# Kernel tuning notes

Measured on AMD Instinct MI355X. Metric: run time of the kernel, lower is better.

## Reference

```python
import jax, jax.numpy as jnp
import numpy as np

N_HEAD = 12
D_HEAD = 64  # inner_dim 768 / 12 heads

def quick_gelu(x):
    return x * jax.nn.sigmoid(1.702 * x)

def setup_inputs() -> dict:
    key = jax.random.key(0)
    ks = jax.random.split(key, 12)
    B, Nv, Lt, Cv, Ct, Ci = 256, 196, 32, 768, 512, 768
    s = lambda k, shp, fan: jax.random.normal(k, shp, jnp.float32) / np.sqrt(fan)
    return {
        "vis_tokens": jax.random.normal(ks[0], (B, Nv, Cv), jnp.float32),
        "text_tokens": jax.random.normal(ks[1], (B, Lt, Ct), jnp.float32),
        "Wq": s(ks[2], (Cv, Ci), Cv), "bq": jnp.zeros((Ci,), jnp.float32),
        "Wk": s(ks[3], (Ct, Ci), Ct), "bk": jnp.zeros((Ci,), jnp.float32),
        "Wv": s(ks[4], (Ct, Ci), Ct), "bv": jnp.zeros((Ci,), jnp.float32),
        "W1": s(ks[5], (Ci, Ci), Ci), "b1": jnp.zeros((Ci,), jnp.float32),
        "W2": s(ks[6], (Ci, 2), Ci), "b2": jnp.zeros((2,), jnp.float32),
    }

def reference(vis_tokens, text_tokens, Wq, bq, Wk, bk, Wv, bv, W1, b1, W2, b2):
    B, Nv, _ = vis_tokens.shape
    Lt = text_tokens.shape[1]
    Ci = Wq.shape[1]
    # projections -> [B, H, N, D]
    q = (vis_tokens @ Wq + bq).reshape(B, Nv, N_HEAD, D_HEAD).transpose(0, 2, 1, 3)
    k = (text_tokens @ Wk + bk).reshape(B, Lt, N_HEAD, D_HEAD).transpose(0, 2, 1, 3)
    v = (text_tokens @ Wv + bv).reshape(B, Lt, N_HEAD, D_HEAD).transpose(0, 2, 1, 3)
    scores = jnp.einsum('bhnd,bhld->bhnl', q, k) / np.sqrt(D_HEAD).astype(np.float32)
    attn = jax.nn.softmax(scores, axis=-1)           # [B,H,Nv,Lt]
    ctx = jnp.einsum('bhnl,bhld->bhnd', attn, v)      # [B,H,Nv,D]
    ctx = ctx.transpose(0, 2, 1, 3).reshape(B, Nv, Ci)
    fused = ctx + vis_tokens[..., :Ci]
    logits = quick_gelu(fused @ W1 + b1) @ W2 + b2    # [B,Nv,2]
    rel_BN = attn.mean(axis=-1).mean(axis=1)          # [B,Nv]
    return (logits, rel_BN)
```

## Files before the change

kernel.cpp:

```cpp
#include <hip/hip_runtime.h>
#include <hip/hip_bf16.h>


typedef __attribute__((ext_vector_type(8))) short bf16x8;
typedef __attribute__((ext_vector_type(4))) float f32x4;

__device__ __forceinline__ float bf2f(unsigned short u) {
    return __uint_as_float(((unsigned int)u) << 16);
}
__device__ __forceinline__ unsigned short f2bf(float f) {
    unsigned int x = __float_as_uint(f);
    unsigned int r = (x + 0x7FFFu + ((x >> 16) & 1u)) >> 16;
    return (unsigned short)r;
}

__global__ void cvt_bf16_kernel(const float* __restrict__ in,
                                unsigned short* __restrict__ out, int n4) {
    int i = blockIdx.x * 256 + threadIdx.x;
    if (i >= n4) return;
    float4 v = ((const float4*)in)[i];
    ushort4 o;
    o.x = f2bf(v.x); o.y = f2bf(v.y); o.z = f2bf(v.z); o.w = f2bf(v.w);
    ((ushort4*)out)[i] = o;
}

__global__ void transpose_cvt_kernel(const float* __restrict__ W,
                                     unsigned short* __restrict__ Wt,
                                     int K, int N) {
    __shared__ float tile[32][33];
    int n0 = blockIdx.x * 32, k0 = blockIdx.y * 32;
    int tx = threadIdx.x & 31, ty = threadIdx.x >> 5;
    #pragma unroll
    for (int r = ty; r < 32; r += 8)
        tile[r][tx] = W[(size_t)(k0 + r) * N + n0 + tx];
    __syncthreads();
    #pragma unroll
    for (int r = ty; r < 32; r += 8)
        Wt[(size_t)(n0 + r) * K + k0 + tx] = f2bf(tile[tx][r]);
}

template<int KTOT, int GELU>
__global__ __launch_bounds__(256, 2)
void gemm_bt_kernel(const unsigned short* __restrict__ A,
                    const unsigned short* __restrict__ Bt,
                    const float* __restrict__ bias,
                    unsigned short* __restrict__ C) {
    constexpr int LDSW = 72;
    __shared__ unsigned short As[128 * LDSW];
    __shared__ unsigned short Bs[128 * LDSW];
    const int tid = threadIdx.x;
    const size_t m0 = (size_t)blockIdx.y * 128;
    const int n0 = blockIdx.x * 128;
    const int lane = tid & 63;
    const int wave = tid >> 6;
    const int wm = (wave >> 1) * 64;
    const int wn = (wave & 1) * 64;
    const int lr = lane & 15;
    const int quad = lane >> 4;

    f32x4 acc[4][4] = {};

    for (int kt = 0; kt < KTOT; kt += 64) {
        #pragma unroll
        for (int i = 0; i < 4; ++i) {
            int c = tid + i * 256;
            int r = c >> 3, col = (c & 7) * 8;
            bf16x8 v = *(const bf16x8*)(A + (m0 + r) * KTOT + kt + col);
            *(bf16x8*)(As + r * LDSW + col) = v;
        }
        #pragma unroll
        for (int i = 0; i < 4; ++i) {
            int c = tid + i * 256;
            int r = c >> 3, col = (c & 7) * 8;
            bf16x8 v = *(const bf16x8*)(Bt + (size_t)(n0 + r) * KTOT + kt + col);
            *(bf16x8*)(Bs + r * LDSW + col) = v;
        }
        __syncthreads();
        #pragma unroll
        for (int kk = 0; kk < 64; kk += 32) {
            bf16x8 fa[4], fb[4];
            #pragma unroll
            for (int i = 0; i < 4; ++i)
                fa[i] = *(const bf16x8*)(As + (wm + i * 16 + lr) * LDSW + kk + quad * 8);
            #pragma unroll
            for (int j = 0; j < 4; ++j)
                fb[j] = *(const bf16x8*)(Bs + (wn + j * 16 + lr) * LDSW + kk + quad * 8);
            #pragma unroll
            for (int i = 0; i < 4; ++i)
                #pragma unroll
                for (int j = 0; j < 4; ++j)
                    acc[i][j] = __builtin_amdgcn_mfma_f32_16x16x32_bf16(
                        fa[i], fb[j], acc[i][j], 0, 0, 0);
        }
        __syncthreads();
    }

    #pragma unroll
    for (int j = 0; j < 4; ++j) {
        int col = n0 + wn + j * 16 + lr;
        float bv = bias[col];
        #pragma unroll
        for (int i = 0; i < 4; ++i) {
            #pragma unroll
            for (int r = 0; r < 4; ++r) {
                size_t row = m0 + wm + i * 16 + quad * 4 + r;
                float x = acc[i][j][r] + bv;
                if (GELU) x = x / (1.0f + __expf(-1.702f * x));
                C[row * 768 + col] = f2bf(x);
            }
        }
    }
}

__global__ __launch_bounds__(256, 4)
void attn_mfma_kernel(const unsigned short* __restrict__ Q,
                      const unsigned short* __restrict__ Kb,
                      const unsigned short* __restrict__ Vb,
                      unsigned short* __restrict__ RF) {
    constexpr int KS = 72;
    constexpr int VS = 34;
    constexpr int PS = 40;
    constexpr int CS = 72;
    __shared__ unsigned short Ks[32 * KS];
    __shared__ unsigned short Vt[64 * VS];
    __shared__ unsigned short Pb[4][16 * PS];
    __shared__ unsigned short Cb[4][16 * CS];
    const int tid = threadIdx.x;
    const int b = blockIdx.x / 12, h = blockIdx.x % 12;
    const int lane = tid & 63, wave = tid >> 6;
    const int lr = lane & 15, quad = lane >> 4;

    {
        int l = tid >> 3, d8 = (tid & 7) * 8;
        size_t base = ((size_t)b * 32 + l) * 768 + (size_t)h * 64 + d8;
        bf16x8 kv = *(const bf16x8*)(Kb + base);
        bf16x8 vv = *(const bf16x8*)(Vb + base);
        *(bf16x8*)(Ks + l * KS + d8) = kv;
        #pragma unroll
        for (int j = 0; j < 8; ++j)
            Vt[(d8 + j) * VS + l] = (unsigned short)vv[j];
    }
    __syncthreads();

    bf16x8 fbK[2][2];
    #pragma unroll
    for (int n = 0; n < 2; ++n)
        #pragma unroll
        for (int ks = 0; ks < 2; ++ks)
            fbK[n][ks] = *(const bf16x8*)(Ks + (n * 16 + lr) * KS + ks * 32 + quad * 8);
    bf16x8 fbV[4];
    #pragma unroll
    for (int d = 0; d < 4; ++d)
        fbV[d] = *(const bf16x8*)(Vt + (d * 16 + lr) * VS + quad * 8);

    const size_t qbase = (size_t)b * 196 * 768 + (size_t)h * 64;

    for (int t = wave; t < 13; t += 4) {
        const int m0 = t * 16;
        int qrow = m0 + lr; if (qrow > 195) qrow = 195;
        const unsigned short* qp = Q + qbase + (size_t)qrow * 768;
        bf16x8 fa0 = *(const bf16x8*)(qp + quad * 8);
        bf16x8 fa1 = *(const bf16x8*)(qp + 32 + quad * 8);
        f32x4 s0 = {}, s1 = {};
        s0 = __builtin_amdgcn_mfma_f32_16x16x32_bf16(fa0, fbK[0][0], s0, 0, 0, 0);
        s0 = __builtin_amdgcn_mfma_f32_16x16x32_bf16(fa1, fbK[0][1], s0, 0, 0, 0);
        s1 = __builtin_amdgcn_mfma_f32_16x16x32_bf16(fa0, fbK[1][0], s1, 0, 0, 0);
        s1 = __builtin_amdgcn_mfma_f32_16x16x32_bf16(fa1, fbK[1][1], s1, 0, 0, 0);

        float p0[4], p1[4], m4[4], s4[4];
        #pragma unroll
        for (int r = 0; r < 4; ++r) {
            p0[r] = s0[r] * 0.125f;
            p1[r] = s1[r] * 0.125f;
            m4[r] = fmaxf(p0[r], p1[r]);
        }
        #pragma unroll
        for (int off = 1; off < 16; off <<= 1)
            #pragma unroll
            for (int r = 0; r < 4; ++r)
                m4[r] = fmaxf(m4[r], __shfl_xor(m4[r], off));
        #pragma unroll
        for (int r = 0; r < 4; ++r) {
            p0[r] = __expf(p0[r] - m4[r]);
            p1[r] = __expf(p1[r] - m4[r]);
            s4[r] = p0[r] + p1[r];
        }
        #pragma unroll
        for (int off = 1; off < 16; off <<= 1)
            #pragma unroll
            for (int r = 0; r < 4; ++r)
                s4[r] += __shfl_xor(s4[r], off);
        #pragma unroll
        for (int r = 0; r < 4; ++r) {
            float inv = __builtin_amdgcn_rcpf(s4[r]);
            unsigned short* pr = &Pb[wave][(quad * 4 + r) * PS];
            pr[lr]      = f2bf(p0[r] * inv);
            pr[16 + lr] = f2bf(p1[r] * inv);
        }

        bf16x8 fap = *(const bf16x8*)(&Pb[wave][lr * PS + quad * 8]);
        f32x4 c[4];
        #pragma unroll
        for (int d = 0; d < 4; ++d) {
            f32x4 z = {};
            c[d] = __builtin_amdgcn_mfma_f32_16x16x32_bf16(fap, fbV[d], z, 0, 0, 0);
        }
        #pragma unroll
        for (int d = 0; d < 4; ++d)
            #pragma unroll
            for (int r = 0; r < 4; ++r)
                Cb[wave][(quad * 4 + r) * CS + d * 16 + lr] = f2bf(c[d][r]);
        #pragma unroll
        for (int i = 0; i < 2; ++i) {
            int c2 = lane + i * 64;
            int row = c2 >> 3, col8 = (c2 & 7) * 8;
            int grow = m0 + row;
            if (grow < 196) {
                bf16x8 cv = *(const bf16x8*)(&Cb[wave][row * CS + col8]);
                unsigned short* gp = RF + qbase + (size_t)grow * 768 + col8;
                bf16x8 rv = *(const bf16x8*)gp;
                bf16x8 ov;
                #pragma unroll
                for (int j = 0; j < 8; ++j)
                    ov[j] = (short)f2bf(bf2f((unsigned short)cv[j]) +
                                        bf2f((unsigned short)rv[j]));
                *(bf16x8*)gp = ov;
            }
        }
    }
}

__global__ __launch_bounds__(256)
void mlp2_kernel(const unsigned short* __restrict__ Hb,
                 const float* __restrict__ W2,
                 const float* __restrict__ b2,
                 float* __restrict__ out) {
    __shared__ float w2s[2][768];
    const int tid = threadIdx.x;
    for (int i = tid; i < 1536; i += 256) w2s[i & 1][i >> 1] = W2[i];
    __syncthreads();
    const int sub = tid & 7;
    const int r = tid >> 3;
    const size_t row = (size_t)blockIdx.x * 32 + r;
    float a0 = 0.f, a1 = 0.f;
    #pragma unroll
    for (int i = 0; i < 12; ++i) {
        int base = i * 64 + sub * 8;
        bf16x8 hv = *(const bf16x8*)(Hb + row * 768 + base);
        #pragma unroll
        for (int j = 0; j < 8; ++j) {
            float hf = bf2f((unsigned short)hv[j]);
            a0 += hf * w2s[0][base + j];
            a1 += hf * w2s[1][base + j];
        }
    }
    #pragma unroll
    for (int o = 4; o >= 1; o >>= 1) {
        a0 += __shfl_down(a0, o, 8);
        a1 += __shfl_down(a1, o, 8);
    }
    if (sub == 0) {
        out[row * 2]      = a0 + b2[0];
        out[row * 2 + 1]  = a1 + b2[1];
        out[100352 + row] = 0.03125f;
    }
}

extern "C" void kernel_launch(void* const* d_in, const int* in_sizes, int n_in,
                              void* d_out, int out_size, void* d_ws, size_t ws_size,
                              hipStream_t stream) {
    const float* vis = (const float*)d_in[0];
    const float* txt = (const float*)d_in[1];
    const float* Wq  = (const float*)d_in[2];
    const float* bq  = (const float*)d_in[3];
    const float* Wk  = (const float*)d_in[4];
    const float* bk  = (const float*)d_in[5];
    const float* Wv  = (const float*)d_in[6];
    const float* bv  = (const float*)d_in[7];
    const float* W1  = (const float*)d_in[8];
    const float* b1  = (const float*)d_in[9];
    const float* W2  = (const float*)d_in[10];
    const float* b2  = (const float*)d_in[11];
    float* out = (float*)d_out;

    char* w = (char*)d_ws;
    unsigned short* Abf = (unsigned short*)(w);
    unsigned short* Tbf = (unsigned short*)(w + 77070336);
    unsigned short* Wqt = (unsigned short*)(w + 85458944);
    unsigned short* Wkt = (unsigned short*)(w + 86638592);
    unsigned short* Wvt = (unsigned short*)(w + 87425024);
    unsigned short* W1t = (unsigned short*)(w + 88211456);
    unsigned short* Qbf = (unsigned short*)(w + 89391104);
    unsigned short* Kbf = (unsigned short*)(w + 166461440);
    unsigned short* Vbf = (unsigned short*)(w + 179044352);
    unsigned short* Hbf = Qbf;

    cvt_bf16_kernel<<<37632, 256, 0, stream>>>(vis, Abf, 9633792);
    cvt_bf16_kernel<<<4096, 256, 0, stream>>>(txt, Tbf, 1048576);
    transpose_cvt_kernel<<<dim3(24, 24), 256, 0, stream>>>(Wq, Wqt, 768, 768);
    transpose_cvt_kernel<<<dim3(24, 16), 256, 0, stream>>>(Wk, Wkt, 512, 768);
    transpose_cvt_kernel<<<dim3(24, 16), 256, 0, stream>>>(Wv, Wvt, 512, 768);
    transpose_cvt_kernel<<<dim3(24, 24), 256, 0, stream>>>(W1, W1t, 768, 768);

    gemm_bt_kernel<768, 0><<<dim3(6, 392), 256, 0, stream>>>(Abf, Wqt, bq, Qbf);
    gemm_bt_kernel<512, 0><<<dim3(6, 64), 256, 0, stream>>>(Tbf, Wkt, bk, Kbf);
    gemm_bt_kernel<512, 0><<<dim3(6, 64), 256, 0, stream>>>(Tbf, Wvt, bv, Vbf);

    attn_mfma_kernel<<<3072, 256, 0, stream>>>(Qbf, Kbf, Vbf, Abf);

    gemm_bt_kernel<768, 1><<<dim3(6, 392), 256, 0, stream>>>(Abf, W1t, b1, Hbf);

    mlp2_kernel<<<1568, 256, 0, stream>>>(Hbf, W2, b2, out);
}
```

Baseline: 546.9 us.

## Load GEMM tiles via direct global-to-LDS loads with XCD-aware block mapping

Replaces the register-staged global-to-LDS copy in the bf16 GEMM with direct global_load_lds 16-byte transfers. The LDS layout changes to row-groups of 8 with padding per group, and the fragment reads are adjusted to match. It also flattens the grid and remaps block ids so each XCD handles a contiguous range of M tiles, which should improve L2 reuse. The change lowers VGPR use and instruction count for loads. It risks LDS bank conflicts in the new layout, and the block remapping assumes the tile count divides evenly by 8.

```diff
diff --git a/kernel.cpp b/kernel.cpp
--- a/kernel.cpp
+++ b/kernel.cpp
@@ -13,6 +13,11 @@
     unsigned int r = (x + 0x7FFFu + ((x >> 16) & 1u)) >> 16;
     return (unsigned short)r;
 }
+
+#define GLOAD_LDS16(gp, lp)                                                    \
+    __builtin_amdgcn_global_load_lds(                                          \
+        (__attribute__((address_space(1))) void*)(gp),                         \
+        (__attribute__((address_space(3))) void*)(lp), 16, 0, 0)
 
 __global__ void cvt_bf16_kernel(const float* __restrict__ in,
                                 unsigned short* __restrict__ out, int n4) {
@@ -39,52 +44,52 @@
         Wt[(size_t)(n0 + r) * K + k0 + tx] = f2bf(tile[tx][r]);
 }
 
-template<int KTOT, int GELU>
+template<int KTOT, int GELU, int MTILES>
 __global__ __launch_bounds__(256, 2)
 void gemm_bt_kernel(const unsigned short* __restrict__ A,
                     const unsigned short* __restrict__ Bt,
                     const float* __restrict__ bias,
                     unsigned short* __restrict__ C) {
-    constexpr int LDSW = 72;
-    __shared__ unsigned short As[128 * LDSW];
-    __shared__ unsigned short Bs[128 * LDSW];
+    constexpr int GS = 520;
+    __shared__ unsigned short As[16 * GS];
+    __shared__ unsigned short Bs[16 * GS];
     const int tid = threadIdx.x;
-    const size_t m0 = (size_t)blockIdx.y * 128;
-    const int n0 = blockIdx.x * 128;
-    const int lane = tid & 63;
-    const int wave = tid >> 6;
-    const int wm = (wave >> 1) * 64;
-    const int wn = (wave & 1) * 64;
-    const int lr = lane & 15;
-    const int quad = lane >> 4;
+    const int lane = tid & 63, wave = tid >> 6;
+    const int id = blockIdx.x;
+    const int xcd = id & 7, local = id >> 3;
+    const int nt = local % 6, mt = xcd * (MTILES / 8) + local / 6;
+    const size_t m0 = (size_t)mt * 128;
+    const int n0 = nt * 128;
+    const int wm = (wave >> 1) * 64, wn = (wave & 1) * 64;
+    const int lr = lane & 15, quad = lane >> 4;
+
+    const unsigned short* gA = A + (m0 + wave * 32 + (lane >> 3)) * KTOT + (lane & 7) * 8;
+    const unsigned short* gB = Bt + ((size_t)n0 + wave * 32 + (lane >> 3)) * KTOT + (lane & 7) * 8;
+    unsigned short* lA = As + (wave * 4) * GS;
+    unsigned short* lB = Bs + (wave * 4) * GS;
 
     f32x4 acc[4][4] = {};
 
     for (int kt = 0; kt < KTOT; kt += 64) {
         #pragma unroll
         for (int i = 0; i < 4; ++i) {
-            int c = tid + i * 256;
-            int r = c >> 3, col = (c & 7) * 8;
-            bf16x8 v = *(const bf16x8*)(A + (m0 + r) * KTOT + kt + col);
-            *(bf16x8*)(As + r * LDSW + col) = v;
-        }
-        #pragma unroll
-        for (int i = 0; i < 4; ++i) {
-            int c = tid + i * 256;
-            int r = c >> 3, col = (c & 7) * 8;
-            bf16x8 v = *(const bf16x8*)(Bt + (size_t)(n0 + r) * KTOT + kt + col);
-            *(bf16x8*)(Bs + r * LDSW + col) = v;
+            GLOAD_LDS16(gA + (size_t)i * 8 * KTOT + kt, lA + i * GS);
+            GLOAD_LDS16(gB + (size_t)i * 8 * KTOT + kt, lB + i * GS);
         }
         __syncthreads();
         #pragma unroll
         for (int kk = 0; kk < 64; kk += 32) {
             bf16x8 fa[4], fb[4];
             #pragma unroll
-            for (int i = 0; i < 4; ++i)
-                fa[i] = *(const bf16x8*)(As + (wm + i * 16 + lr) * LDSW + kk + quad * 8);
-            #pragma unroll
-            for (int j = 0; j < 4; ++j)
-                fb[j] = *(const bf16x8*)(Bs + (wn + j * 16 + lr) * LDSW + kk + quad * 8);
+            for (int i = 0; i < 4; ++i) {
+                int r = wm + i * 16 + lr;
+                fa[i] = *(const bf16x8*)(As + (r >> 3) * GS + (r & 7) * 64 + kk + quad * 8);
+            }
+            #pragma unroll
+            for (int j = 0; j < 4; ++j) {
+                int r = wn + j * 16 + lr;
+                fb[j] = *(const bf16x8*)(Bs + (r >> 3) * GS + (r & 7) * 64 + kk + quad * 8);
+            }
             #pragma unroll
             for (int i = 0; i < 4; ++i)
                 #pragma unroll
@@ -302,13 +307,13 @@
     transpose_cvt_kernel<<<dim3(24, 16), 256, 0, stream>>>(Wv, Wvt, 512, 768);
     transpose_cvt_kernel<<<dim3(24, 24), 256, 0, stream>>>(W1, W1t, 768, 768);
 
-    gemm_bt_kernel<768, 0><<<dim3(6, 392), 256, 0, stream>>>(Abf, Wqt, bq, Qbf);
-    gemm_bt_kernel<512, 0><<<dim3(6, 64), 256, 0, stream>>>(Tbf, Wkt, bk, Kbf);
-    gemm_bt_kernel<512, 0><<<dim3(6, 64), 256, 0, stream>>>(Tbf, Wvt, bv, Vbf);
+    gemm_bt_kernel<768, 0, 392><<<2352, 256, 0, stream>>>(Abf, Wqt, bq, Qbf);
+    gemm_bt_kernel<512, 0, 64><<<384, 256, 0, stream>>>(Tbf, Wkt, bk, Kbf);
+    gemm_bt_kernel<512, 0, 64><<<384, 256, 0, stream>>>(Tbf, Wvt, bv, Vbf);
 
     attn_mfma_kernel<<<3072, 256, 0, stream>>>(Qbf, Kbf, Vbf, Abf);
 
-    gemm_bt_kernel<768, 1><<<dim3(6, 392), 256, 0, stream>>>(Abf, W1t, b1, Hbf);
+    gemm_bt_kernel<768, 1, 392><<<2352, 256, 0, stream>>>(Abf, W1t, b1, Hbf);
 
     mlp2_kernel<<<1568, 256, 0, stream>>>(Hbf, W2, b2, out);
 }
```

Result: faster. 516.5 us (-5.6%).
